# Kernel tuning notes

Hardware: AMD Instinct MI355X
Metric: run time of the kernel (lower is better)

## Reference

```python
import jax, jax.numpy as jnp
import numpy as np

B, T, D, H = 2, 2048, 1024, 16
DH = D // H


def setup_inputs() -> dict:
    key = jax.random.key(0)
    ks = jax.random.split(key, 8)
    s = 1.0 / np.sqrt(D)  # xavier-ish scale
    return {
        "query": jax.random.normal(ks[0], (B, T, D), jnp.float32),
        "key": jax.random.normal(ks[1], (B, T, D), jnp.float32),
        "value": jax.random.normal(ks[2], (B, T, D), jnp.float32),
        "Wq": jax.random.normal(ks[3], (D, D), jnp.float32) * s,
        "bq": jnp.zeros((D,), jnp.float32),
        "Wk": jax.random.normal(ks[4], (D, D), jnp.float32) * s,
        "bk": jnp.zeros((D,), jnp.float32),
        "Wv": jax.random.normal(ks[5], (D, D), jnp.float32) * s,
        "bv": jnp.zeros((D,), jnp.float32),
        "Wo": jax.random.normal(ks[6], (D, D), jnp.float32) * s,
        "bo": jnp.zeros((D,), jnp.float32),
        # causal mask (B, T, T); True = attend
        "mask": jnp.broadcast_to(jnp.tril(jnp.ones((T, T), bool)), (B, T, T)),
    }


def _split_heads(x):  # (B, T, D) -> (B, H, T, Dh)
    return x.reshape(B, T, H, DH).transpose(0, 2, 1, 3)


def reference(query, key, value, Wq, bq, Wk, bk, Wv, bv, Wo, bo, mask):
    q = _split_heads(query @ Wq + bq)
    k = _split_heads(key @ Wk + bk)
    v = _split_heads(value @ Wv + bv)
    scores = jnp.einsum("bhqd,bhkd->bhqk", q, k) / jnp.sqrt(jnp.float32(DH))
    scores = jnp.where(mask[:, None, :, :], scores, -jnp.inf)
    w = jax.nn.softmax(scores, axis=-1)
    out = jnp.einsum("bhqk,bhkd->bhqd", w, v)
    out = out.transpose(0, 2, 1, 3).reshape(B, T, D)  # merge heads
    return out @ Wo + bo
```

## Files before the change

### kernel.cpp

```cpp
#include <hip/hip_runtime.h>

typedef unsigned short u16;
typedef __attribute__((ext_vector_type(4))) float f32x4;
typedef __attribute__((ext_vector_type(8))) short bf16x8;

#define MFMA16(a,b,c) __builtin_amdgcn_mfma_f32_16x16x32_bf16((a),(b),(c),0,0,0)

__device__ inline u16 f2bf(float f){
  union { float f; unsigned u; } v; v.f = f;
  unsigned r = v.u + 0x7FFFu + ((v.u >> 16) & 1u);
  return (u16)(r >> 16);
}
__device__ inline u16 f2bf_fast(float f){
  union { float f; unsigned u; } v; v.f = f;
  return (u16)((v.u + 0x8000u) >> 16);
}
__device__ inline void storeC(float* p, float v){ *p = v; }
__device__ inline void storeC(u16* p, float v){ *p = f2bf(v); }

typedef const __attribute__((address_space(1))) unsigned int* gas_ptr;
typedef __attribute__((address_space(3))) unsigned int* las_ptr;
__device__ inline void gload_lds16(const u16* g, u16* l){
  __builtin_amdgcn_global_load_lds((gas_ptr)(const void*)g, (las_ptr)(void*)l, 16, 0, 0);
}

template<int N>
__device__ inline float rorf(float v){
  union { float f; int i; } a, b; a.f = v;
  b.i = __builtin_amdgcn_update_dpp(a.i, a.i, 0x120|N, 0xF, 0xF, false);
  return b.f;
}
__device__ inline float redMax16(float v){
  v = fmaxf(v, rorf<8>(v)); v = fmaxf(v, rorf<4>(v));
  v = fmaxf(v, rorf<2>(v)); v = fmaxf(v, rorf<1>(v));
  return v;
}

struct CvtArgs { const float* x[3]; u16* y[3]; };
__global__ void k_cvt3(CvtArgs a, int n4){
  const float* x = a.x[blockIdx.y];
  u16* y = a.y[blockIdx.y];
  int i = blockIdx.x*blockDim.x + threadIdx.x;
  if (i < n4){
    float4 v = ((const float4*)x)[i];
    ushort4 o;
    o.x = f2bf(v.x); o.y = f2bf(v.y); o.z = f2bf(v.z); o.w = f2bf(v.w);
    ((ushort4*)y)[i] = o;
  }
}

struct TwbArgs { const float* W[4]; u16* Wt[4]; };
__global__ void k_twb4(TwbArgs a){
  __shared__ u16 t[32][33];
  const float* W = a.W[blockIdx.z];
  u16* Wt = a.Wt[blockIdx.z];
  int kb = blockIdx.x*32, nb = blockIdx.y*32;
  int tx = threadIdx.x, ty = threadIdx.y;
  #pragma unroll
  for (int i=0;i<32;i+=8)
    t[ty+i][tx] = f2bf(W[(size_t)(kb+ty+i)*1024 + nb+tx]);
  __syncthreads();
  #pragma unroll
  for (int i=0;i<32;i+=8)
    Wt[(size_t)(nb+ty+i)*1024 + kb+tx] = t[tx][ty+i];
}

__global__ void k_tv(const u16* __restrict__ V, u16* __restrict__ VT){
  __shared__ u16 t[32][33];
  int tb = blockIdx.x*32;
  int db = blockIdx.y*32;
  int bh = blockIdx.z;
  int b = bh>>4, h = bh&15;
  int tx = threadIdx.x, ty = threadIdx.y;
  #pragma unroll
  for (int i=0;i<32;i+=8)
    t[ty+i][tx] = V[(size_t)(b*2048 + tb+ty+i)*1024 + h*64 + db+tx];
  __syncthreads();
  #pragma unroll
  for (int i=0;i<32;i+=8)
    VT[(size_t)(bh*64 + db+ty+i)*2048 + tb+tx] = t[tx][ty+i];
}

template<typename OutT>
__device__ inline void gemm_body(const u16* __restrict__ A, const u16* __restrict__ Bt,
                                 const float* __restrict__ bias, OutT* __restrict__ C,
                                 int bx, int by){
  const int N=1024, K=1024;
  __shared__ __attribute__((aligned(16))) u16 As[128*64];
  __shared__ __attribute__((aligned(16))) u16 Bs[128*64];
  const int tid  = threadIdx.x;
  const int wave = tid>>6, lane = tid&63;
  const int lo = lane&15, hi = lane>>4;
  const int row0 = bx*128, col0 = by*128;
  const int wm = (wave>>1)*64, wn = (wave&1)*64;
  f32x4 acc[4][4];
  #pragma unroll
  for (int i=0;i<4;i++)
    #pragma unroll
    for (int j=0;j<4;j++) acc[i][j] = (f32x4){0.f,0.f,0.f,0.f};

  for (int k0=0; k0<K; k0+=64){
    #pragma unroll
    for (int r=0;r<4;r++){
      int c = r*256 + tid;
      gload_lds16(A  + (size_t)(row0 + (c>>3))*K + k0 + (c&7)*8, As + c*8);
      gload_lds16(Bt + (size_t)(col0 + (c>>3))*K + k0 + (c&7)*8, Bs + c*8);
    }
    __syncthreads();
    __builtin_amdgcn_s_setprio(1);
    #pragma unroll
    for (int ks=0;ks<2;ks++){
      bf16x8 af[4], bfr[4];
      #pragma unroll
      for (int mf=0;mf<4;mf++)
        af[mf] = *(const bf16x8*)(As + (wm+mf*16+lo)*64 + ks*32 + hi*8);
      #pragma unroll
      for (int nf=0;nf<4;nf++)
        bfr[nf] = *(const bf16x8*)(Bs + (wn+nf*16+lo)*64 + ks*32 + hi*8);
      #pragma unroll
      for (int mf=0;mf<4;mf++)
        #pragma unroll
        for (int nf=0;nf<4;nf++)
          acc[mf][nf] = MFMA16(af[mf], bfr[nf], acc[mf][nf]);
    }
    __builtin_amdgcn_s_setprio(0);
    __syncthreads();
  }
  #pragma unroll
  for (int mf=0;mf<4;mf++){
    #pragma unroll
    for (int nf=0;nf<4;nf++){
      int r0 = row0 + wm + mf*16 + hi*4;
      int c0 = col0 + wn + nf*16 + lo;
      float bb = bias[c0];
      #pragma unroll
      for (int r=0;r<4;r++)
        storeC(&C[(size_t)(r0+r)*N + c0], acc[mf][nf][r] + bb);
    }
  }
}

struct GemmArgs3 { const u16* A[3]; const u16* Bt[3]; const float* bias[3]; u16* C[3]; };
__global__ __launch_bounds__(256) void k_gemm3(GemmArgs3 g){
  int flat = blockIdx.x + (blockIdx.y<<5) + (blockIdx.z<<8);
  int swz = (flat&7)*96 + (flat>>3);
  int by = swz & 7, bx = (swz>>3) & 31, bz = swz >> 8;
  gemm_body<u16>(g.A[bz], g.Bt[bz], g.bias[bz], g.C[bz], bx, by);
}
__global__ __launch_bounds__(256) void k_gemmO(const u16* __restrict__ A, const u16* __restrict__ Bt,
                                               const float* __restrict__ bias, float* __restrict__ C){
  int flat = blockIdx.x + (blockIdx.y<<5);
  int swz = (flat&7)*32 + (flat>>3);
  int by = swz & 7, bx = swz >> 3;
  gemm_body<float>(A, Bt, bias, C, bx, by);
}

__global__ __launch_bounds__(256) void k_attn(
    const u16* __restrict__ Q, const u16* __restrict__ Kp,
    const u16* __restrict__ VT, u16* __restrict__ O)
{
  const int T=2048, D=1024;
  __shared__ __attribute__((aligned(16))) u16 Ks[2][64*64];
  __shared__ __attribute__((aligned(16))) u16 Vs[2][64*64];
  __shared__ __attribute__((aligned(16))) u16 Plds[4][16*64];
  int f = blockIdx.x + (blockIdx.y<<5);
  int xcd = f & 7, idx = f >> 3;
  const int bh = (xcd<<2) | (idx&3);
  const int qb = 31 - (idx>>2);
  const int b = bh>>4, h = bh&15;
  const int tid = threadIdx.x;
  const int wave = tid>>6, lane = tid&63;
  const int lo = lane&15, hi = lane>>4;
  const float NEG = -__builtin_inff();
  const float sc = 0.125f * 1.44269504f;
  const bf16x8 ones = {0x3F80,0x3F80,0x3F80,0x3F80,0x3F80,0x3F80,0x3F80,0x3F80};

  const int cof0 = ((hi    ) ^ (lo&7))*8;
  const int cof1 = ((hi + 4) ^ (lo&7))*8;

  const int c0 = tid, c1 = 256 + tid;
  const int sr0 = c0>>3, sj0 = (c0&7)^(sr0&7);
  const int sr1 = c1>>3, sj1 = (c1&7)^(sr1&7);
  const u16* Kbase = Kp + (size_t)(b*T)*D + h*64;
  const u16* Vbase = VT + (size_t)(bh*64)*T;
  const size_t kOff0 = (size_t)sr0*D + sj0*8, kOff1 = (size_t)sr1*D + sj1*8;
  const size_t vOff0 = (size_t)sr0*T + sj0*8, vOff1 = (size_t)sr1*T + sj1*8;

  const int qrow0 = qb*64 + wave*16;
  const u16* Qb = Q + (size_t)(b*T + qrow0 + lo)*D + h*64;
  bf16x8 qf0 = *(const bf16x8*)(Qb + hi*8);
  bf16x8 qf1 = *(const bf16x8*)(Qb + 32 + hi*8);

  f32x4 o[4];
  #pragma unroll
  for (int nf=0;nf<4;nf++) o[nf] = (f32x4){0.f,0.f,0.f,0.f};
  float m[4], l[4];
  #pragma unroll
  for (int r=0;r<4;r++){ m[r] = NEG; l[r] = 0.f; }

  gload_lds16(Kbase + kOff0, &Ks[0][c0*8]);
  gload_lds16(Kbase + kOff1, &Ks[0][c1*8]);
  gload_lds16(Vbase + vOff0, &Vs[0][c0*8]);
  gload_lds16(Vbase + vOff1, &Vs[0][c1*8]);
  __syncthreads();

  int cur = 0;
  for (int kb=0; kb<=qb; kb++){
    if (kb < qb){
      const u16* Kt = Kbase + (size_t)(kb+1)*64*D;
      const u16* Vt = Vbase + (kb+1)*64;
      gload_lds16(Kt + kOff0, &Ks[cur^1][c0*8]);
      gload_lds16(Kt + kOff1, &Ks[cur^1][c1*8]);
      gload_lds16(Vt + vOff0, &Vs[cur^1][c0*8]);
      gload_lds16(Vt + vOff1, &Vs[cur^1][c1*8]);
    }
    const u16* Kl = Ks[cur];
    const u16* Vl = Vs[cur];
    f32x4 s[4];
    __builtin_amdgcn_s_setprio(1);
    #pragma unroll
    for (int nf=0;nf<4;nf++){
      int row = nf*16 + lo;
      bf16x8 kf0 = *(const bf16x8*)(Kl + row*64 + cof0);
      bf16x8 kf1 = *(const bf16x8*)(Kl + row*64 + cof1);
      f32x4 z = (f32x4){0.f,0.f,0.f,0.f};
      z = MFMA16(qf0, kf0, z);
      s[nf] = MFMA16(qf1, kf1, z);
    }
    __builtin_amdgcn_s_setprio(0);
    float pm[4] = {NEG,NEG,NEG,NEG};
    if (kb == qb){
      #pragma unroll
      for (int nf=0;nf<4;nf++){
        int col = kb*64 + nf*16 + lo;
        #pragma unroll
        for (int r=0;r<4;r++){
          int row = qrow0 + hi*4 + r;
          if (col > row) s[nf][r] = NEG;
          pm[r] = fmaxf(pm[r], s[nf][r]);
        }
      }
    } else {
      #pragma unroll
      for (int nf=0;nf<4;nf++)
        #pragma unroll
        for (int r=0;r<4;r++)
          pm[r] = fmaxf(pm[r], s[nf][r]);
    }
    #pragma unroll
    for (int r=0;r<4;r++) pm[r] = redMax16(pm[r]);
    bool small = true;
    #pragma unroll
    for (int r=0;r<4;r++) small = small && (pm[r] <= m[r] + 44.f);
    const bool resc = !__all(small);
    float alpha[4];
    if (resc){
      #pragma unroll
      for (int r=0;r<4;r++){
        float mn = fmaxf(m[r], pm[r]);
        alpha[r] = __builtin_amdgcn_exp2f((m[r] - mn)*sc);
        m[r] = mn;
      }
      #pragma unroll
      for (int nf=0;nf<4;nf++)
        #pragma unroll
        for (int r=0;r<4;r++) o[nf][r] *= alpha[r];
    }
    float msc[4];
    #pragma unroll
    for (int r=0;r<4;r++) msc[r] = m[r]*sc;
    #pragma unroll
    for (int nf=0;nf<4;nf++)
      #pragma unroll
      for (int r=0;r<4;r++){
        float p = __builtin_amdgcn_exp2f(__builtin_fmaf(s[nf][r], sc, -msc[r]));
        int prow = hi*4+r, pcol = nf*16+lo;
        Plds[wave][prow*64 + (pcol ^ ((prow&7)<<3))] = f2bf_fast(p);
      }
    bf16x8 pa0 = *(const bf16x8*)(&Plds[wave][lo*64 + cof0]);
    bf16x8 pa1 = *(const bf16x8*)(&Plds[wave][lo*64 + cof1]);
    f32x4 lsum = (f32x4){0.f,0.f,0.f,0.f};
    __builtin_amdgcn_s_setprio(1);
    lsum = MFMA16(pa0, ones, lsum);
    lsum = MFMA16(pa1, ones, lsum);
    #pragma unroll
    for (int nf=0;nf<4;nf++){
      int row = nf*16 + lo;
      bf16x8 v0 = *(const bf16x8*)(Vl + row*64 + cof0);
      bf16x8 v1 = *(const bf16x8*)(Vl + row*64 + cof1);
      o[nf] = MFMA16(pa0, v0, o[nf]);
      o[nf] = MFMA16(pa1, v1, o[nf]);
    }
    __builtin_amdgcn_s_setprio(0);
    if (resc){
      #pragma unroll
      for (int r=0;r<4;r++) l[r] = l[r]*alpha[r] + lsum[r];
    } else {
      #pragma unroll
      for (int r=0;r<4;r++) l[r] += lsum[r];
    }
    __syncthreads();
    cur ^= 1;
  }
  #pragma unroll
  for (int nf=0;nf<4;nf++)
    #pragma unroll
    for (int r=0;r<4;r++){
      int row = qrow0 + hi*4 + r;
      O[(size_t)(b*T+row)*D + h*64 + nf*16 + lo] = f2bf_fast(o[nf][r] / l[r]);
    }
}

extern "C" void kernel_launch(void* const* d_in, const int* in_sizes, int n_in,
                              void* d_out, int out_size, void* d_ws, size_t ws_size,
                              hipStream_t stream) {
  const int B=2, T=2048, D=1024;
  const int M = B*T;
  const float* query = (const float*)d_in[0];
  const float* key   = (const float*)d_in[1];
  const float* value = (const float*)d_in[2];
  const float* Wq = (const float*)d_in[3];  const float* bq = (const float*)d_in[4];
  const float* Wk = (const float*)d_in[5];  const float* bk = (const float*)d_in[6];
  const float* Wv = (const float*)d_in[7];  const float* bv = (const float*)d_in[8];
  const float* Wo = (const float*)d_in[9];  const float* bo = (const float*)d_in[10];
  float* out = (float*)d_out;

  char* ws = (char*)d_ws;
  const size_t MB = 1024*1024;
  u16* xq  = (u16*)(ws + 0*MB);
  u16* xk  = (u16*)(ws + 8*MB);
  u16* xv  = (u16*)(ws + 16*MB);
  u16* WqT = (u16*)(ws + 24*MB);
  u16* WkT = (u16*)(ws + 26*MB);
  u16* WvT = (u16*)(ws + 28*MB);
  u16* WoT = (u16*)(ws + 30*MB);
  u16* Qp  = (u16*)(ws + 32*MB);
  u16* Kp  = (u16*)(ws + 40*MB);
  u16* Vp  = (u16*)(ws + 48*MB);
  u16* VTp = (u16*)(ws + 56*MB);
  u16* AO  = (u16*)(ws + 64*MB);

  int n4 = M*D/4;
  CvtArgs ca; ca.x[0]=query; ca.x[1]=key; ca.x[2]=value; ca.y[0]=xq; ca.y[1]=xk; ca.y[2]=xv;
  k_cvt3<<<dim3(n4/256, 3), 256, 0, stream>>>(ca, n4);

  TwbArgs ta; ta.W[0]=Wq; ta.W[1]=Wk; ta.W[2]=Wv; ta.W[3]=Wo;
  ta.Wt[0]=WqT; ta.Wt[1]=WkT; ta.Wt[2]=WvT; ta.Wt[3]=WoT;
  k_twb4<<<dim3(32,32,4), dim3(32,8), 0, stream>>>(ta);

  GemmArgs3 ga;
  ga.A[0]=xq; ga.A[1]=xk; ga.A[2]=xv;
  ga.Bt[0]=WqT; ga.Bt[1]=WkT; ga.Bt[2]=WvT;
  ga.bias[0]=bq; ga.bias[1]=bk; ga.bias[2]=bv;
  ga.C[0]=Qp; ga.C[1]=Kp; ga.C[2]=Vp;
  k_gemm3<<<dim3(32,8,3), 256, 0, stream>>>(ga);

  k_tv<<<dim3(T/32, 2, 32), dim3(32,8), 0, stream>>>(Vp, VTp);
  k_attn<<<dim3(32,32), 256, 0, stream>>>(Qp, Kp, VTp, AO);
  k_gemmO<<<dim3(32,8), 256, 0, stream>>>(AO, WoT, bo, out);
}
```

Before: 132.3 us.

## Fuse V transpose into QKV GEMM epilogue, widen attention blocks, shrink output GEMM tiles

The V projection GEMM now writes its output directly in per-head transposed layout, which removes the separate transpose kernel and its extra global round trip. The attention kernel uses 512-thread blocks covering 128 query rows, so each K/V tile loaded into LDS serves twice as many waves. Waves whose diagonal block is already done skip compute but still take part in the barriers. The output GEMM uses 64x128 tiles on a 512-block grid with XCD-aware mapping, to spread the work over more CUs at some cost in per-block reuse.

```diff
diff --git a/kernel.cpp b/kernel.cpp
--- a/kernel.cpp
+++ b/kernel.cpp
@@ -15,8 +15,6 @@
   union { float f; unsigned u; } v; v.f = f;
   return (u16)((v.u + 0x8000u) >> 16);
 }
-__device__ inline void storeC(float* p, float v){ *p = v; }
-__device__ inline void storeC(u16* p, float v){ *p = f2bf(v); }
 
 typedef const __attribute__((address_space(1))) unsigned int* gas_ptr;
 typedef __attribute__((address_space(3))) unsigned int* las_ptr;
@@ -65,27 +63,14 @@
     Wt[(size_t)(nb+ty+i)*1024 + kb+tx] = t[tx][ty+i];
 }
 
-__global__ void k_tv(const u16* __restrict__ V, u16* __restrict__ VT){
-  __shared__ u16 t[32][33];
-  int tb = blockIdx.x*32;
-  int db = blockIdx.y*32;
-  int bh = blockIdx.z;
-  int b = bh>>4, h = bh&15;
-  int tx = threadIdx.x, ty = threadIdx.y;
-  #pragma unroll
-  for (int i=0;i<32;i+=8)
-    t[ty+i][tx] = V[(size_t)(b*2048 + tb+ty+i)*1024 + h*64 + db+tx];
-  __syncthreads();
-  #pragma unroll
-  for (int i=0;i<32;i+=8)
-    VT[(size_t)(bh*64 + db+ty+i)*2048 + tb+tx] = t[tx][ty+i];
-}
-
-template<typename OutT>
-__device__ inline void gemm_body(const u16* __restrict__ A, const u16* __restrict__ Bt,
-                                 const float* __restrict__ bias, OutT* __restrict__ C,
-                                 int bx, int by){
+struct GemmArgs3 { const u16* A[3]; const u16* Bt[3]; const float* bias[3]; u16* C[3]; };
+__global__ __launch_bounds__(256) void k_gemm3(GemmArgs3 g){
   const int N=1024, K=1024;
+  int flat = blockIdx.x + (blockIdx.y<<5) + (blockIdx.z<<8);
+  int swz = (flat&7)*96 + (flat>>3);
+  int by = swz & 7, bx = (swz>>3) & 31, bz = swz >> 8;
+  const u16* A = g.A[bz]; const u16* Bt = g.Bt[bz];
+  const float* bias = g.bias[bz]; u16* C = g.C[bz];
   __shared__ __attribute__((aligned(16))) u16 As[128*64];
   __shared__ __attribute__((aligned(16))) u16 Bs[128*64];
   const int tid  = threadIdx.x;
@@ -126,47 +111,116 @@
     __builtin_amdgcn_s_setprio(0);
     __syncthreads();
   }
-  #pragma unroll
-  for (int mf=0;mf<4;mf++){
+  if (bz == 2){
+    #pragma unroll
+    for (int mf=0;mf<4;mf++){
+      #pragma unroll
+      for (int nf=0;nf<4;nf++){
+        int c0 = col0 + wn + nf*16 + lo;
+        int hh = c0>>6, dh = c0&63;
+        int r0 = row0 + wm + mf*16 + hi*4;
+        int bb = r0>>11, tt = r0&2047;
+        float bv = bias[c0];
+        ushort4 pk;
+        pk.x = f2bf(acc[mf][nf][0]+bv);
+        pk.y = f2bf(acc[mf][nf][1]+bv);
+        pk.z = f2bf(acc[mf][nf][2]+bv);
+        pk.w = f2bf(acc[mf][nf][3]+bv);
+        *(ushort4*)(C + ((size_t)((bb*16+hh)*64+dh))*2048 + tt) = pk;
+      }
+    }
+  } else {
+    #pragma unroll
+    for (int mf=0;mf<4;mf++){
+      #pragma unroll
+      for (int nf=0;nf<4;nf++){
+        int r0 = row0 + wm + mf*16 + hi*4;
+        int c0 = col0 + wn + nf*16 + lo;
+        float bv = bias[c0];
+        #pragma unroll
+        for (int r=0;r<4;r++)
+          C[(size_t)(r0+r)*N + c0] = f2bf(acc[mf][nf][r] + bv);
+      }
+    }
+  }
+}
+
+__global__ __launch_bounds__(256) void k_gemmO(const u16* __restrict__ A, const u16* __restrict__ Bt,
+                                               const float* __restrict__ bias, float* __restrict__ C){
+  const int N=1024, K=1024;
+  int f = blockIdx.x;
+  int xcd = f & 7, idx = f >> 3;
+  int bx = xcd*8 + (idx>>3), by = idx & 7;
+  __shared__ __attribute__((aligned(16))) u16 As[64*64];
+  __shared__ __attribute__((aligned(16))) u16 Bs[128*64];
+  const int tid  = threadIdx.x;
+  const int wave = tid>>6, lane = tid&63;
+  const int lo = lane&15, hi = lane>>4;
+  const int row0 = bx*64, col0 = by*128;
+  const int wm = (wave>>1)*32, wn = (wave&1)*64;
+  f32x4 acc[2][4];
+  #pragma unroll
+  for (int i=0;i<2;i++)
+    #pragma unroll
+    for (int j=0;j<4;j++) acc[i][j] = (f32x4){0.f,0.f,0.f,0.f};
+
+  for (int k0=0; k0<K; k0+=64){
+    #pragma unroll
+    for (int r=0;r<2;r++){
+      int c = r*256 + tid;
+      gload_lds16(A + (size_t)(row0 + (c>>3))*K + k0 + (c&7)*8, As + c*8);
+    }
+    #pragma unroll
+    for (int r=0;r<4;r++){
+      int c = r*256 + tid;
+      gload_lds16(Bt + (size_t)(col0 + (c>>3))*K + k0 + (c&7)*8, Bs + c*8);
+    }
+    __syncthreads();
+    __builtin_amdgcn_s_setprio(1);
+    #pragma unroll
+    for (int ks=0;ks<2;ks++){
+      bf16x8 af[2], bfr[4];
+      #pragma unroll
+      for (int mf=0;mf<2;mf++)
+        af[mf] = *(const bf16x8*)(As + (wm+mf*16+lo)*64 + ks*32 + hi*8);
+      #pragma unroll
+      for (int nf=0;nf<4;nf++)
+        bfr[nf] = *(const bf16x8*)(Bs + (wn+nf*16+lo)*64 + ks*32 + hi*8);
+      #pragma unroll
+      for (int mf=0;mf<2;mf++)
+        #pragma unroll
+        for (int nf=0;nf<4;nf++)
+          acc[mf][nf] = MFMA16(af[mf], bfr[nf], acc[mf][nf]);
+    }
+    __builtin_amdgcn_s_setprio(0);
+    __syncthreads();
+  }
+  #pragma unroll
+  for (int mf=0;mf<2;mf++){
     #pragma unroll
     for (int nf=0;nf<4;nf++){
       int r0 = row0 + wm + mf*16 + hi*4;
       int c0 = col0 + wn + nf*16 + lo;
-      float bb = bias[c0];
+      float bv = bias[c0];
       #pragma unroll
       for (int r=0;r<4;r++)
-        storeC(&C[(size_t)(r0+r)*N + c0], acc[mf][nf][r] + bb);
-    }
-  }
-}
-
-struct GemmArgs3 { const u16* A[3]; const u16* Bt[3]; const float* bias[3]; u16* C[3]; };
-__global__ __launch_bounds__(256) void k_gemm3(GemmArgs3 g){
-  int flat = blockIdx.x + (blockIdx.y<<5) + (blockIdx.z<<8);
-  int swz = (flat&7)*96 + (flat>>3);
-  int by = swz & 7, bx = (swz>>3) & 31, bz = swz >> 8;
-  gemm_body<u16>(g.A[bz], g.Bt[bz], g.bias[bz], g.C[bz], bx, by);
-}
-__global__ __launch_bounds__(256) void k_gemmO(const u16* __restrict__ A, const u16* __restrict__ Bt,
-                                               const float* __restrict__ bias, float* __restrict__ C){
-  int flat = blockIdx.x + (blockIdx.y<<5);
-  int swz = (flat&7)*32 + (flat>>3);
-  int by = swz & 7, bx = swz >> 3;
-  gemm_body<float>(A, Bt, bias, C, bx, by);
-}
-
-__global__ __launch_bounds__(256) void k_attn(
+        C[(size_t)(r0+r)*N + c0] = acc[mf][nf][r] + bv;
+    }
+  }
+}
+
+__global__ __launch_bounds__(512) void k_attn(
     const u16* __restrict__ Q, const u16* __restrict__ Kp,
     const u16* __restrict__ VT, u16* __restrict__ O)
 {
   const int T=2048, D=1024;
   __shared__ __attribute__((aligned(16))) u16 Ks[2][64*64];
   __shared__ __attribute__((aligned(16))) u16 Vs[2][64*64];
-  __shared__ __attribute__((aligned(16))) u16 Plds[4][16*64];
-  int f = blockIdx.x + (blockIdx.y<<5);
+  __shared__ __attribute__((aligned(16))) u16 Plds[8][16*64];
+  int f = blockIdx.x;
   int xcd = f & 7, idx = f >> 3;
-  const int bh = (xcd<<2) | (idx&3);
-  const int qb = 31 - (idx>>2);
+  const int bh  = (xcd<<2) | (idx&3);
+  const int qb2 = 15 - (idx>>2);
   const int b = bh>>4, h = bh&15;
   const int tid = threadIdx.x;
   const int wave = tid>>6, lane = tid&63;
@@ -175,18 +229,19 @@
   const float sc = 0.125f * 1.44269504f;
   const bf16x8 ones = {0x3F80,0x3F80,0x3F80,0x3F80,0x3F80,0x3F80,0x3F80,0x3F80};
 
+  const int kbmax = 2*qb2 + 1;
+  const int kb_d  = 2*qb2 + (wave>>2);
+
   const int cof0 = ((hi    ) ^ (lo&7))*8;
   const int cof1 = ((hi + 4) ^ (lo&7))*8;
 
-  const int c0 = tid, c1 = 256 + tid;
-  const int sr0 = c0>>3, sj0 = (c0&7)^(sr0&7);
-  const int sr1 = c1>>3, sj1 = (c1&7)^(sr1&7);
+  const int sr = tid>>3, sj = (tid&7)^(sr&7);
   const u16* Kbase = Kp + (size_t)(b*T)*D + h*64;
   const u16* Vbase = VT + (size_t)(bh*64)*T;
-  const size_t kOff0 = (size_t)sr0*D + sj0*8, kOff1 = (size_t)sr1*D + sj1*8;
-  const size_t vOff0 = (size_t)sr0*T + sj0*8, vOff1 = (size_t)sr1*T + sj1*8;
-
-  const int qrow0 = qb*64 + wave*16;
+  const size_t kOff = (size_t)sr*D + sj*8;
+  const size_t vOff = (size_t)sr*T + sj*8;
+
+  const int qrow0 = qb2*128 + wave*16;
   const u16* Qb = Q + (size_t)(b*T + qrow0 + lo)*D + h*64;
   bf16x8 qf0 = *(const bf16x8*)(Qb + hi*8);
   bf16x8 qf1 = *(const bf16x8*)(Qb + 32 + hi*8);
@@ -198,106 +253,104 @@
   #pragma unroll
   for (int r=0;r<4;r++){ m[r] = NEG; l[r] = 0.f; }
 
-  gload_lds16(Kbase + kOff0, &Ks[0][c0*8]);
-  gload_lds16(Kbase + kOff1, &Ks[0][c1*8]);
-  gload_lds16(Vbase + vOff0, &Vs[0][c0*8]);
-  gload_lds16(Vbase + vOff1, &Vs[0][c1*8]);
+  gload_lds16(Kbase + kOff, &Ks[0][tid*8]);
+  gload_lds16(Vbase + vOff, &Vs[0][tid*8]);
   __syncthreads();
 
   int cur = 0;
-  for (int kb=0; kb<=qb; kb++){
-    if (kb < qb){
+  for (int kb=0; kb<=kbmax; kb++){
+    if (kb < kbmax){
       const u16* Kt = Kbase + (size_t)(kb+1)*64*D;
       const u16* Vt = Vbase + (kb+1)*64;
-      gload_lds16(Kt + kOff0, &Ks[cur^1][c0*8]);
-      gload_lds16(Kt + kOff1, &Ks[cur^1][c1*8]);
-      gload_lds16(Vt + vOff0, &Vs[cur^1][c0*8]);
-      gload_lds16(Vt + vOff1, &Vs[cur^1][c1*8]);
-    }
-    const u16* Kl = Ks[cur];
-    const u16* Vl = Vs[cur];
-    f32x4 s[4];
-    __builtin_amdgcn_s_setprio(1);
-    #pragma unroll
-    for (int nf=0;nf<4;nf++){
-      int row = nf*16 + lo;
-      bf16x8 kf0 = *(const bf16x8*)(Kl + row*64 + cof0);
-      bf16x8 kf1 = *(const bf16x8*)(Kl + row*64 + cof1);
-      f32x4 z = (f32x4){0.f,0.f,0.f,0.f};
-      z = MFMA16(qf0, kf0, z);
-      s[nf] = MFMA16(qf1, kf1, z);
-    }
-    __builtin_amdgcn_s_setprio(0);
-    float pm[4] = {NEG,NEG,NEG,NEG};
-    if (kb == qb){
+      gload_lds16(Kt + kOff, &Ks[cur^1][tid*8]);
+      gload_lds16(Vt + vOff, &Vs[cur^1][tid*8]);
+    }
+    if (kb <= kb_d){
+      const u16* Kl = Ks[cur];
+      const u16* Vl = Vs[cur];
+      f32x4 s[4];
+      __builtin_amdgcn_s_setprio(1);
       #pragma unroll
       for (int nf=0;nf<4;nf++){
-        int col = kb*64 + nf*16 + lo;
+        int row = nf*16 + lo;
+        bf16x8 kf0 = *(const bf16x8*)(Kl + row*64 + cof0);
+        bf16x8 kf1 = *(const bf16x8*)(Kl + row*64 + cof1);
+        f32x4 z = (f32x4){0.f,0.f,0.f,0.f};
+        z = MFMA16(qf0, kf0, z);
+        s[nf] = MFMA16(qf1, kf1, z);
+      }
+      __builtin_amdgcn_s_setprio(0);
+      float pm[4] = {NEG,NEG,NEG,NEG};
+      if (kb == kb_d){
+        #pragma unroll
+        for (int nf=0;nf<4;nf++){
+          int col = kb*64 + nf*16 + lo;
+          #pragma unroll
+          for (int r=0;r<4;r++){
+            int row = qrow0 + hi*4 + r;
+            if (col > row) s[nf][r] = NEG;
+            pm[r] = fmaxf(pm[r], s[nf][r]);
+          }
+        }
+      } else {
+        #pragma unroll
+        for (int nf=0;nf<4;nf++)
+          #pragma unroll
+          for (int r=0;r<4;r++)
+            pm[r] = fmaxf(pm[r], s[nf][r]);
+      }
+      #pragma unroll
+      for (int r=0;r<4;r++) pm[r] = redMax16(pm[r]);
+      bool small = true;
+      #pragma unroll
+      for (int r=0;r<4;r++) small = small && (pm[r] <= m[r] + 44.f);
+      const bool resc = !__all(small);
+      float alpha[4];
+      if (resc){
         #pragma unroll
         for (int r=0;r<4;r++){
-          int row = qrow0 + hi*4 + r;
-          if (col > row) s[nf][r] = NEG;
-          pm[r] = fmaxf(pm[r], s[nf][r]);
+          float mn = fmaxf(m[r], pm[r]);
+          alpha[r] = __builtin_amdgcn_exp2f((m[r] - mn)*sc);
+          m[r] = mn;
         }
-      }
-    } else {
+        #pragma unroll
+        for (int nf=0;nf<4;nf++)
+          #pragma unroll
+          for (int r=0;r<4;r++) o[nf][r] *= alpha[r];
+      }
+      float msc[4];
+      #pragma unroll
+      for (int r=0;r<4;r++) msc[r] = m[r]*sc;
       #pragma unroll
       for (int nf=0;nf<4;nf++)
         #pragma unroll
-        for (int r=0;r<4;r++)
-          pm[r] = fmaxf(pm[r], s[nf][r]);
-    }
-    #pragma unroll
-    for (int r=0;r<4;r++) pm[r] = redMax16(pm[r]);
-    bool small = true;
-    #pragma unroll
-    for (int r=0;r<4;r++) small = small && (pm[r] <= m[r] + 44.f);
-    const bool resc = !__all(small);
-    float alpha[4];
-    if (resc){
-      #pragma unroll
-      for (int r=0;r<4;r++){
-        float mn = fmaxf(m[r], pm[r]);
-        alpha[r] = __builtin_amdgcn_exp2f((m[r] - mn)*sc);
-        m[r] = mn;
-      }
-      #pragma unroll
-      for (int nf=0;nf<4;nf++)
-        #pragma unroll
-        for (int r=0;r<4;r++) o[nf][r] *= alpha[r];
-    }
-    float msc[4];
-    #pragma unroll
-    for (int r=0;r<4;r++) msc[r] = m[r]*sc;
-    #pragma unroll
-    for (int nf=0;nf<4;nf++)
-      #pragma unroll
-      for (int r=0;r<4;r++){
-        float p = __builtin_amdgcn_exp2f(__builtin_fmaf(s[nf][r], sc, -msc[r]));
-        int prow = hi*4+r, pcol = nf*16+lo;
-        Plds[wave][prow*64 + (pcol ^ ((prow&7)<<3))] = f2bf_fast(p);
-      }
-    bf16x8 pa0 = *(const bf16x8*)(&Plds[wave][lo*64 + cof0]);
-    bf16x8 pa1 = *(const bf16x8*)(&Plds[wave][lo*64 + cof1]);
-    f32x4 lsum = (f32x4){0.f,0.f,0.f,0.f};
-    __builtin_amdgcn_s_setprio(1);
-    lsum = MFMA16(pa0, ones, lsum);
-    lsum = MFMA16(pa1, ones, lsum);
-    #pragma unroll
-    for (int nf=0;nf<4;nf++){
-      int row = nf*16 + lo;
-      bf16x8 v0 = *(const bf16x8*)(Vl + row*64 + cof0);
-      bf16x8 v1 = *(const bf16x8*)(Vl + row*64 + cof1);
-      o[nf] = MFMA16(pa0, v0, o[nf]);
-      o[nf] = MFMA16(pa1, v1, o[nf]);
-    }
-    __builtin_amdgcn_s_setprio(0);
-    if (resc){
-      #pragma unroll
-      for (int r=0;r<4;r++) l[r] = l[r]*alpha[r] + lsum[r];
-    } else {
-      #pragma unroll
-      for (int r=0;r<4;r++) l[r] += lsum[r];
+        for (int r=0;r<4;r++){
+          float p = __builtin_amdgcn_exp2f(__builtin_fmaf(s[nf][r], sc, -msc[r]));
+          int prow = hi*4+r, pcol = nf*16+lo;
+          Plds[wave][prow*64 + (pcol ^ ((prow&7)<<3))] = f2bf_fast(p);
+        }
+      bf16x8 pa0 = *(const bf16x8*)(&Plds[wave][lo*64 + cof0]);
+      bf16x8 pa1 = *(const bf16x8*)(&Plds[wave][lo*64 + cof1]);
+      f32x4 lsum = (f32x4){0.f,0.f,0.f,0.f};
+      __builtin_amdgcn_s_setprio(1);
+      lsum = MFMA16(pa0, ones, lsum);
+      lsum = MFMA16(pa1, ones, lsum);
+      #pragma unroll
+      for (int nf=0;nf<4;nf++){
+        int row = nf*16 + lo;
+        bf16x8 v0 = *(const bf16x8*)(Vl + row*64 + cof0);
+        bf16x8 v1 = *(const bf16x8*)(Vl + row*64 + cof1);
+        o[nf] = MFMA16(pa0, v0, o[nf]);
+        o[nf] = MFMA16(pa1, v1, o[nf]);
+      }
+      __builtin_amdgcn_s_setprio(0);
+      if (resc){
+        #pragma unroll
+        for (int r=0;r<4;r++) l[r] = l[r]*alpha[r] + lsum[r];
+      } else {
+        #pragma unroll
+        for (int r=0;r<4;r++) l[r] += lsum[r];
+      }
     }
     __syncthreads();
     cur ^= 1;
@@ -336,7 +389,6 @@
   u16* WoT = (u16*)(ws + 30*MB);
   u16* Qp  = (u16*)(ws + 32*MB);
   u16* Kp  = (u16*)(ws + 40*MB);
-  u16* Vp  = (u16*)(ws + 48*MB);
   u16* VTp = (u16*)(ws + 56*MB);
   u16* AO  = (u16*)(ws + 64*MB);
 
@@ -352,10 +404,9 @@
   ga.A[0]=xq; ga.A[1]=xk; ga.A[2]=xv;
   ga.Bt[0]=WqT; ga.Bt[1]=WkT; ga.Bt[2]=WvT;
   ga.bias[0]=bq; ga.bias[1]=bk; ga.bias[2]=bv;
-  ga.C[0]=Qp; ga.C[1]=Kp; ga.C[2]=Vp;
+  ga.C[0]=Qp; ga.C[1]=Kp; ga.C[2]=VTp;
   k_gemm3<<<dim3(32,8,3), 256, 0, stream>>>(ga);
 
-  k_tv<<<dim3(T/32, 2, 32), dim3(32,8), 0, stream>>>(Vp, VTp);
-  k_attn<<<dim3(32,32), 256, 0, stream>>>(Qp, Kp, VTp, AO);
-  k_gemmO<<<dim3(32,8), 256, 0, stream>>>(AO, WoT, bo, out);
-}
+  k_attn<<<512, 512, 0, stream>>>(Qp, Kp, VTp, AO);
+  k_gemmO<<<512, 256, 0, stream>>>(AO, WoT, bo, out);
+}
```

Measured after the change: 150.0 us. +13.4%, slower.
